# Kernel tuning notes

Measured on AMD Instinct MI355X. Metric: run time of the kernel, lower is better.

Reference implementation:

```python
import jax, jax.numpy as jnp
import numpy as np

N_NODES = 10000
N_EDGES = 640000
D = 128            # node_dims == edge_dims
HID = 2 * D        # ff hidden
EPS = 1e-6


def _layernorm(x, g, b):
    mu = jnp.mean(x, axis=-1, keepdims=True)
    var = jnp.var(x, axis=-1, keepdims=True)
    return (x - mu) * jax.lax.rsqrt(var + EPS) * g + b


def setup_inputs() -> dict:
    key = jax.random.key(0)
    ks = jax.random.split(key, 16)
    def lin(k, fan_in, fan_out):
        lim = 1.0 / np.sqrt(fan_in)
        kw, kb = jax.random.split(k)
        W = jax.random.uniform(kw, (fan_in, fan_out), jnp.float32, -lim, lim)
        b = jax.random.uniform(kb, (fan_out,), jnp.float32, -lim, lim)
        return W, b
    x = jax.random.normal(ks[0], (N_NODES, D), jnp.float32)
    edge_index = jax.random.randint(ks[1], (2, N_EDGES), 0, N_NODES, jnp.int64)
    edge_attr = jax.random.normal(ks[2], (N_EDGES, D), jnp.float32)
    # message MLP: Linear(3D->D), ReLU, Linear(D->D), ReLU, Linear(D->D)
    W1, b1 = lin(ks[3], 3 * D, D)
    W2, b2 = lin(ks[4], D, D)
    W3, b3 = lin(ks[5], D, D)
    # feedforward: Linear(D->2D), ReLU, Linear(2D->D)
    F1, bf1 = lin(ks[6], D, HID)
    F2, bf2 = lin(ks[7], HID, D)
    g0 = jnp.ones((D,), jnp.float32); be0 = jnp.zeros((D,), jnp.float32)
    g1 = jnp.ones((D,), jnp.float32); be1 = jnp.zeros((D,), jnp.float32)
    return {"x": x, "edge_index": edge_index, "edge_attr": edge_attr,
            "W1": W1, "b1": b1, "W2": W2, "b2": b2, "W3": W3, "b3": b3,
            "F1": F1, "bf1": bf1, "F2": F2, "bf2": bf2,
            "g0": g0, "be0": be0, "g1": g1, "be1": be1}


def reference(x, edge_index, edge_attr, W1, b1, W2, b2, W3, b3,
              F1, bf1, F2, bf2, g0, be0, g1, be1):
    src = edge_index[0]  # j
    dst = edge_index[1]  # i
    # message: cat([h_V_i, edge_attr, h_V_j]) -> MLP  (E x 3D gather)
    m = jnp.concatenate([x[dst], edge_attr, x[src]], axis=-1)
    m = jax.nn.relu(m @ W1 + b1)
    m = jax.nn.relu(m @ W2 + b2)
    m = m @ W3 + b3  # [E, D]
    # scatter-mean over destination nodes
    sums = jax.ops.segment_sum(m, dst, num_segments=N_NODES)
    cnt = jax.ops.segment_sum(jnp.ones((N_EDGES,), m.dtype), dst, num_segments=N_NODES)
    dh = sums / jnp.maximum(cnt, 1.0)[:, None]
    # residual + norm (dropout is identity at inference)
    h = _layernorm(x + dh, g0, be0)
    # pointwise feedforward
    ff = jax.nn.relu(h @ F1 + bf1) @ F2 + bf2
    return _layernorm(h + ff, g1, be1)
```

## Files before the change

### kernel.cpp

```cpp
#include <hip/hip_runtime.h>


#define NE 640000
#define NN 10000
#define DD 128
#define HIDN 256
#define EPSF 1e-6f
#define TILES4 10
#define EBLK4 250

typedef __attribute__((ext_vector_type(8))) short short8;
typedef __attribute__((ext_vector_type(4))) float f32x4;

__device__ __forceinline__ unsigned short f2bf(float f) {
    union { float f; unsigned int u; } v; v.f = f;
    unsigned int r = v.u + 0x7FFFu + ((v.u >> 16) & 1u);
    return (unsigned short)(r >> 16);
}
__device__ __forceinline__ float bf2f(unsigned short h) {
    union { unsigned int u; float f; } v; v.u = ((unsigned int)h) << 16;
    return v.f;
}
__device__ __forceinline__ int swzcol(int row, int col) {
    return (((col >> 3) ^ (row & 7)) << 3) | (col & 7);
}
__device__ __forceinline__ const short8* frag(const unsigned short* buf,
                                              int row, int kc, int q) {
    int g = (kc * 4 + q) ^ (row & 7);
    return (const short8*)(buf + row * 128 + g * 8);
}

__global__ __launch_bounds__(256)
void prep_pq(const float* __restrict__ W1, const float* __restrict__ W2,
             const float* __restrict__ W3, const float* __restrict__ b1,
             const float* __restrict__ x,
             unsigned short* __restrict__ WT,
             unsigned short* __restrict__ Pp, unsigned short* __restrict__ Qp)
{
    const int t = threadIdx.x;
    if (blockIdx.x < 192) {
        int g = blockIdx.x * 256 + t;
        int layer = g >> 14, r = g & 16383;
        int n = r >> 7, k = r & 127;
        const float* W = (layer == 0) ? (W1 + 128 * DD) : (layer == 1 ? W2 : W3);
        WT[layer * 16384 + n * 128 + swzcol(n, k)] = f2bf(W[k * DD + n]);
        return;
    }
    __shared__ float sx[16][DD];
    const int nb = (blockIdx.x - 192) * 16;

#pragma unroll
    for (int p = 0; p < 2; ++p) {
        int f = t + p * 256;
        int row = f >> 5, c4 = (f & 31) << 2;
        *(float4*)&sx[row][c4] = *(const float4*)(x + (long)(nb + row) * DD + c4);
    }
    __syncthreads();

    const int j  = t & 127;
    const int g8 = (t >> 7) << 3;
    const int pj = ((j & 15) << 3) + (j >> 4);

    for (int pass = 0; pass < 2; ++pass) {
        const float* W = W1 + (pass ? 256 * DD : 0);
        float acc[8];
#pragma unroll
        for (int v = 0; v < 8; ++v) acc[v] = 0.f;
        for (int k4 = 0; k4 < DD; k4 += 4) {
            float w0 = W[(k4 + 0) * DD + j];
            float w1 = W[(k4 + 1) * DD + j];
            float w2 = W[(k4 + 2) * DD + j];
            float w3 = W[(k4 + 3) * DD + j];
#pragma unroll
            for (int v = 0; v < 8; ++v) {
                float4 hv = *(const float4*)&sx[g8 + v][k4];
                acc[v] = fmaf(hv.x, w0, acc[v]);
                acc[v] = fmaf(hv.y, w1, acc[v]);
                acc[v] = fmaf(hv.z, w2, acc[v]);
                acc[v] = fmaf(hv.w, w3, acc[v]);
            }
        }
        unsigned short* Out = pass ? Qp : Pp;
        float bb = pass ? 0.f : b1[j];
#pragma unroll
        for (int v = 0; v < 8; ++v)
            Out[(long)(nb + g8 + v) * 128 + pj] = f2bf(acc[v] + bb);
    }
}

__global__ __launch_bounds__(512, 2)
void edge_mfma(const float* __restrict__ ea, const int* __restrict__ ei,
               const unsigned short* __restrict__ WT,
               const unsigned short* __restrict__ Pp,
               const unsigned short* __restrict__ Qp,
               const float* __restrict__ b2, const float* __restrict__ b3,
               float* __restrict__ sums, float* __restrict__ cnt)
{
    __shared__ unsigned short sW[3 * 16384];
    __shared__ unsigned short sAct[8 * 4096];

    const int t = threadIdx.x;
    const int wave = t >> 6, lane = t & 63;
    const int ln = lane & 15, q = lane >> 4;
    unsigned short* myA = sAct + wave * 4096;

    {
        const uint4* s = (const uint4*)WT;
        uint4* d = (uint4*)sW;
#pragma unroll
        for (int p = 0; p < 12; ++p) d[t + p * 512] = s[t + p * 512];
    }
    __syncthreads();

    float bv2[8], bv3[8];
#pragma unroll
    for (int ct = 0; ct < 8; ++ct) {
        bv2[ct] = b2[ct * 16 + ln];
        bv3[ct] = b3[ct * 16 + ln];
    }

    const long blkbase = (long)blockIdx.x * (TILES4 * 256);

    float4 Aq[16];
    int dstR[8], srcR[8];
    {
        long tb = blkbase;
#pragma unroll
        for (int rt = 0; rt < 2; ++rt)
#pragma unroll
            for (int kc = 0; kc < 4; ++kc) {
                long row = tb + wave * 32 + rt * 16 + ln;
                const float* p = ea + row * DD + kc * 32 + q * 8;
                Aq[rt * 8 + kc * 2 + 0] = *(const float4*)(p);
                Aq[rt * 8 + kc * 2 + 1] = *(const float4*)(p + 4);
            }
#pragma unroll
        for (int r = 0; r < 8; ++r) {
            long row = tb + wave * 32 + (r >> 2) * 16 + q * 4 + (r & 3);
            dstR[r] = ei[(long)NE + row];
            srcR[r] = ei[row];
        }
    }

    for (int it = 0; it < TILES4; ++it) {
        short8 af[2][4];
#pragma unroll
        for (int rt = 0; rt < 2; ++rt)
#pragma unroll
            for (int kc = 0; kc < 4; ++kc) {
                const float* f0 = (const float*)&Aq[rt * 8 + kc * 2];
                short8 v;
#pragma unroll
                for (int jj = 0; jj < 8; ++jj) v[jj] = (short)f2bf(f0[jj]);
                af[rt][kc] = v;
            }

        f32x4 acc[2][8];
#pragma unroll
        for (int r = 0; r < 8; ++r) {
            uint4 pv = *(const uint4*)(Pp + (long)dstR[r] * 128 + ln * 8);
            uint4 qv = *(const uint4*)(Qp + (long)srcR[r] * 128 + ln * 8);
            const unsigned short* pe = (const unsigned short*)&pv;
            const unsigned short* qe = (const unsigned short*)&qv;
#pragma unroll
            for (int ct = 0; ct < 8; ++ct)
                acc[r >> 2][ct][r & 3] = bf2f(pe[ct]) + bf2f(qe[ct]);
        }

        long nb_ = blkbase + (long)((it + 1 < TILES4) ? it + 1 : it) * 256;
        int ndst[8], nsrc[8];
#pragma unroll
        for (int rt = 0; rt < 2; ++rt)
#pragma unroll
            for (int kc = 0; kc < 4; ++kc) {
                long row = nb_ + wave * 32 + rt * 16 + ln;
                const float* p = ea + row * DD + kc * 32 + q * 8;
                Aq[rt * 8 + kc * 2 + 0] = *(const float4*)(p);
                Aq[rt * 8 + kc * 2 + 1] = *(const float4*)(p + 4);
            }
#pragma unroll
        for (int r = 0; r < 8; ++r) {
            long row = nb_ + wave * 32 + (r >> 2) * 16 + q * 4 + (r & 3);
            ndst[r] = ei[(long)NE + row];
            nsrc[r] = ei[row];
        }

#pragma unroll
        for (int kc = 0; kc < 4; ++kc)
#pragma unroll
            for (int ct = 0; ct < 8; ++ct) {
                short8 b = *frag(sW, ct * 16 + ln, kc, q);
                acc[0][ct] = __builtin_amdgcn_mfma_f32_16x16x32_bf16(af[0][kc], b, acc[0][ct], 0, 0, 0);
                acc[1][ct] = __builtin_amdgcn_mfma_f32_16x16x32_bf16(af[1][kc], b, acc[1][ct], 0, 0, 0);
            }
#pragma unroll
        for (int rt = 0; rt < 2; ++rt)
#pragma unroll
            for (int rg = 0; rg < 4; ++rg) {
                int row = rt * 16 + q * 4 + rg;
#pragma unroll
                for (int ct = 0; ct < 8; ++ct) {
                    int col = ct * 16 + ln;
                    myA[row * 128 + swzcol(row, col)] =
                        f2bf(fmaxf(acc[rt][ct][rg], 0.f));
                }
            }
        __builtin_amdgcn_wave_barrier();

#pragma unroll
        for (int rt = 0; rt < 2; ++rt)
#pragma unroll
            for (int ct = 0; ct < 8; ++ct) acc[rt][ct] = (f32x4)(0.f);
#pragma unroll
        for (int kc = 0; kc < 4; ++kc) {
            short8 a0 = *frag(myA, ln, kc, q);
            short8 a1 = *frag(myA, 16 + ln, kc, q);
#pragma unroll
            for (int ct = 0; ct < 8; ++ct) {
                short8 b = *frag(sW + 16384, ct * 16 + ln, kc, q);
                acc[0][ct] = __builtin_amdgcn_mfma_f32_16x16x32_bf16(a0, b, acc[0][ct], 0, 0, 0);
                acc[1][ct] = __builtin_amdgcn_mfma_f32_16x16x32_bf16(a1, b, acc[1][ct], 0, 0, 0);
            }
        }
        __builtin_amdgcn_wave_barrier();
#pragma unroll
        for (int rt = 0; rt < 2; ++rt)
#pragma unroll
            for (int rg = 0; rg < 4; ++rg) {
                int row = rt * 16 + q * 4 + rg;
#pragma unroll
                for (int ct = 0; ct < 8; ++ct) {
                    int col = ct * 16 + ln;
                    myA[row * 128 + swzcol(row, col)] =
                        f2bf(fmaxf(acc[rt][ct][rg] + bv2[ct], 0.f));
                }
            }
        __builtin_amdgcn_wave_barrier();

#pragma unroll
        for (int rt = 0; rt < 2; ++rt)
#pragma unroll
            for (int ct = 0; ct < 8; ++ct) acc[rt][ct] = (f32x4)(0.f);
#pragma unroll
        for (int kc = 0; kc < 4; ++kc) {
            short8 a0 = *frag(myA, ln, kc, q);
            short8 a1 = *frag(myA, 16 + ln, kc, q);
#pragma unroll
            for (int ct = 0; ct < 8; ++ct) {
                short8 b = *frag(sW + 32768, ct * 16 + ln, kc, q);
                acc[0][ct] = __builtin_amdgcn_mfma_f32_16x16x32_bf16(a0, b, acc[0][ct], 0, 0, 0);
                acc[1][ct] = __builtin_amdgcn_mfma_f32_16x16x32_bf16(a1, b, acc[1][ct], 0, 0, 0);
            }
        }
#pragma unroll
        for (int rt = 0; rt < 2; ++rt)
#pragma unroll
            for (int rg = 0; rg < 4; ++rg) {
                long dof = (long)dstR[rt * 4 + rg] * DD;
#pragma unroll
                for (int ct = 0; ct < 8; ++ct)
                    atomicAdd(sums + dof + ct * 16 + ln,
                              acc[rt][ct][rg] + bv3[ct]);
            }
        if (ln == 0) {
#pragma unroll
            for (int r = 0; r < 8; ++r) atomicAdd(cnt + dstR[r], 1.0f);
        }
#pragma unroll
        for (int r = 0; r < 8; ++r) { dstR[r] = ndst[r]; srcR[r] = nsrc[r]; }
    }
}

__global__ __launch_bounds__(256)
void node_fused(const float* __restrict__ x,
                const float* __restrict__ sums, const float* __restrict__ cnt,
                const float* __restrict__ F1, const float* __restrict__ bf1,
                const float* __restrict__ F2, const float* __restrict__ bf2,
                const float* __restrict__ g0, const float* __restrict__ be0,
                const float* __restrict__ g1, const float* __restrict__ be1,
                float* __restrict__ out)
{
    constexpr int NPB = 8;
    __shared__ float sh[NPB][DD];
    __shared__ float shid[NPB][HIDN];
    __shared__ float sz[NPB][DD];

    const int t = threadIdx.x;
    const int wave = t >> 6, lane = t & 63;
    const int half = lane >> 5, l2 = lane & 31;
    const int nl = wave * 2 + half;
    const int node = blockIdx.x * NPB + nl;
    const long base = (long)node * DD;

    float inv = 1.0f / fmaxf(cnt[node], 1.0f);
    float y[4], s = 0.f, ss = 0.f;
#pragma unroll
    for (int e = 0; e < 4; ++e) {
        int c = l2 + 32 * e;
        y[e] = x[base + c] + sums[base + c] * inv;
        s += y[e]; ss += y[e] * y[e];
    }
#pragma unroll
    for (int off = 16; off > 0; off >>= 1) {
        s += __shfl_down(s, off, 32); ss += __shfl_down(ss, off, 32);
    }
    s = __shfl(s, 0, 32); ss = __shfl(ss, 0, 32);
    float mean = s * (1.0f / DD);
    float var  = ss * (1.0f / DD) - mean * mean;
    float rstd = rsqrtf(var + EPSF);
#pragma unroll
    for (int e = 0; e < 4; ++e) {
        int c = l2 + 32 * e;
        sh[nl][c] = (y[e] - mean) * rstd * g0[c] + be0[c];
    }
    __syncthreads();

    float hacc[NPB];
    float bb = bf1[t];
#pragma unroll
    for (int v = 0; v < NPB; ++v) hacc[v] = bb;
    for (int k4 = 0; k4 < DD; k4 += 4) {
        float w0 = F1[(long)(k4 + 0) * HIDN + t];
        float w1 = F1[(long)(k4 + 1) * HIDN + t];
        float w2 = F1[(long)(k4 + 2) * HIDN + t];
        float w3 = F1[(long)(k4 + 3) * HIDN + t];
#pragma unroll
        for (int v = 0; v < NPB; ++v) {
            float4 hv = *(const float4*)&sh[v][k4];
            hacc[v] = fmaf(hv.x, w0, hacc[v]);
            hacc[v] = fmaf(hv.y, w1, hacc[v]);
            hacc[v] = fmaf(hv.z, w2, hacc[v]);
            hacc[v] = fmaf(hv.w, w3, hacc[v]);
        }
    }
#pragma unroll
    for (int v = 0; v < NPB; ++v) shid[v][t] = fmaxf(hacc[v], 0.f);
    __syncthreads();

    const int col = t & (DD - 1);
    const int grp = (t >> 7) * 4;
    float o[4];
#pragma unroll
    for (int v = 0; v < 4; ++v) o[v] = bf2[col];
    for (int k4 = 0; k4 < HIDN; k4 += 4) {
        float w0 = F2[(long)(k4 + 0) * DD + col];
        float w1 = F2[(long)(k4 + 1) * DD + col];
        float w2 = F2[(long)(k4 + 2) * DD + col];
        float w3 = F2[(long)(k4 + 3) * DD + col];
#pragma unroll
        for (int v = 0; v < 4; ++v) {
            float4 hv = *(const float4*)&shid[grp + v][k4];
            o[v] = fmaf(hv.x, w0, o[v]);
            o[v] = fmaf(hv.y, w1, o[v]);
            o[v] = fmaf(hv.z, w2, o[v]);
            o[v] = fmaf(hv.w, w3, o[v]);
        }
    }
#pragma unroll
    for (int v = 0; v < 4; ++v) sz[grp + v][col] = sh[grp + v][col] + o[v];
    __syncthreads();

    float z[4]; s = 0.f; ss = 0.f;
#pragma unroll
    for (int e = 0; e < 4; ++e) {
        int c = l2 + 32 * e;
        z[e] = sz[nl][c]; s += z[e]; ss += z[e] * z[e];
    }
#pragma unroll
    for (int off = 16; off > 0; off >>= 1) {
        s += __shfl_down(s, off, 32); ss += __shfl_down(ss, off, 32);
    }
    s = __shfl(s, 0, 32); ss = __shfl(ss, 0, 32);
    mean = s * (1.0f / DD);
    var  = ss * (1.0f / DD) - mean * mean;
    rstd = rsqrtf(var + EPSF);
#pragma unroll
    for (int e = 0; e < 4; ++e) {
        int c = l2 + 32 * e;
        out[base + c] = (z[e] - mean) * rstd * g1[c] + be1[c];
    }
}

extern "C" void kernel_launch(void* const* d_in, const int* in_sizes, int n_in,
                              void* d_out, int out_size, void* d_ws, size_t ws_size,
                              hipStream_t stream)
{
    const float* x   = (const float*)d_in[0];
    const int*   ei  = (const int*)  d_in[1];
    const float* ea  = (const float*)d_in[2];
    const float* W1  = (const float*)d_in[3];
    const float* b1  = (const float*)d_in[4];
    const float* W2  = (const float*)d_in[5];
    const float* b2  = (const float*)d_in[6];
    const float* W3  = (const float*)d_in[7];
    const float* b3  = (const float*)d_in[8];
    const float* F1  = (const float*)d_in[9];
    const float* bf1 = (const float*)d_in[10];
    const float* F2  = (const float*)d_in[11];
    const float* bf2 = (const float*)d_in[12];
    const float* g0  = (const float*)d_in[13];
    const float* be0 = (const float*)d_in[14];
    const float* g1  = (const float*)d_in[15];
    const float* be1 = (const float*)d_in[16];
    float* out = (float*)d_out;

    char* ws = (char*)d_ws;
    float*          sums = (float*)(ws);
    float*          cnt  = (float*)(ws + 5120000);
    unsigned short* WT   = (unsigned short*)(ws + 5160192);
    unsigned short* Pp   = (unsigned short*)(ws + 5258752);
    unsigned short* Qp   = (unsigned short*)(ws + 7818752);

    hipMemsetAsync(ws, 0, 5160000, stream);
    prep_pq<<<192 + NN / 16, 256, 0, stream>>>(W1, W2, W3, b1, x, WT, Pp, Qp);
    edge_mfma<<<EBLK4, 512, 0, stream>>>(ea, ei, WT, Pp, Qp, b2, b3, sums, cnt);
    node_fused<<<NN / 8, 256, 0, stream>>>(x, sums, cnt, F1, bf1, F2, bf2,
                                           g0, be0, g1, be1, out);
}
```

Measured before the change: 807.9 us.

## Sort edges by destination and merge consecutive same-destination atomics

Adds a counting sort of edges by destination (histogram, single-block scan, scatter) and has the edge kernel process edges in sorted order, gathering edge_attr rows through a permutation. Within each 4-row MFMA fragment group, runs of equal destination are summed in registers before one atomicAdd, and the separate count atomics are replaced by the histogram. The P/Q addition moves into the first-layer epilogue, with the edge features staged through LDS. The goal is less atomic contention and traffic, in exchange for three extra kernel launches, a serial scan, and edge_attr reads that are no longer contiguous.

```diff
diff --git a/kernel.cpp b/kernel.cpp
--- a/kernel.cpp
+++ b/kernel.cpp
@@ -6,8 +6,8 @@
 #define DD 128
 #define HIDN 256
 #define EPSF 1e-6f
-#define TILES4 10
-#define EBLK4 250
+#define TILES5 10
+#define EBLK5 250
 
 typedef __attribute__((ext_vector_type(8))) short short8;
 typedef __attribute__((ext_vector_type(4))) float f32x4;
@@ -57,9 +57,9 @@
     }
     __syncthreads();
 
-    const int j  = t & 127;
+    const int s  = t & 127;
+    const int j  = ((s & 7) << 4) | (s >> 3);
     const int g8 = (t >> 7) << 3;
-    const int pj = ((j & 15) << 3) + (j >> 4);
 
     for (int pass = 0; pass < 2; ++pass) {
         const float* W = W1 + (pass ? 256 * DD : 0);
@@ -84,17 +84,67 @@
         float bb = pass ? 0.f : b1[j];
 #pragma unroll
         for (int v = 0; v < 8; ++v)
-            Out[(long)(nb + g8 + v) * 128 + pj] = f2bf(acc[v] + bb);
-    }
+            Out[(long)(nb + g8 + v) * 128 + s] = f2bf(acc[v] + bb);
+    }
+}
+
+__global__ __launch_bounds__(256)
+void hist_kernel(const int* __restrict__ ei, int* __restrict__ hist)
+{
+    int e = blockIdx.x * 256 + threadIdx.x;
+    atomicAdd(hist + ei[(long)NE + e], 1);
+}
+
+__global__ __launch_bounds__(256)
+void scan_kernel(const int* __restrict__ hist, int* __restrict__ ofs)
+{
+    __shared__ int wsum[4];
+    __shared__ int carry;
+    const int t = threadIdx.x, w = t >> 6, l = t & 63;
+    if (t == 0) carry = 0;
+    __syncthreads();
+    for (int base = 0; base < NN; base += 256) {
+        int v = (base + t < NN) ? hist[base + t] : 0;
+        int inc = v;
+#pragma unroll
+        for (int off = 1; off < 64; off <<= 1) {
+            int u = __shfl_up(inc, off);
+            if (l >= off) inc += u;
+        }
+        if (l == 63) wsum[w] = inc;
+        __syncthreads();
+        int add = 0;
+        for (int i = 0; i < 4; ++i) if (i < w) add += wsum[i];
+        if (base + t < NN) ofs[base + t] = carry + add + inc - v;
+        __syncthreads();
+        if (t == 255) carry += wsum[0] + wsum[1] + wsum[2] + wsum[3];
+        __syncthreads();
+    }
+}
+
+__global__ __launch_bounds__(256)
+void scatter_kernel(const int* __restrict__ ei, int* __restrict__ ofs,
+                    int* __restrict__ permE, int* __restrict__ permSrc,
+                    int* __restrict__ permDst)
+{
+    int e = blockIdx.x * 256 + threadIdx.x;
+    int sN = ei[e];
+    int d  = ei[(long)NE + e];
+    int pos = atomicAdd(ofs + d, 1);
+    permE[pos]   = e;
+    permSrc[pos] = sN;
+    permDst[pos] = d;
 }
 
 __global__ __launch_bounds__(512, 2)
-void edge_mfma(const float* __restrict__ ea, const int* __restrict__ ei,
+void edge_mfma(const float* __restrict__ ea,
+               const int* __restrict__ permE, const int* __restrict__ permSrc,
+               const int* __restrict__ permDst,
                const unsigned short* __restrict__ WT,
                const unsigned short* __restrict__ Pp,
                const unsigned short* __restrict__ Qp,
                const float* __restrict__ b2, const float* __restrict__ b3,
-               float* __restrict__ sums, float* __restrict__ cnt)
+               float* __restrict__ sums)
 {
     __shared__ unsigned short sW[3 * 16384];
     __shared__ unsigned short sAct[8 * 4096];
@@ -102,6 +152,7 @@
     const int t = threadIdx.x;
     const int wave = t >> 6, lane = t & 63;
     const int ln = lane & 15, q = lane >> 4;
+    const int hi = lane >> 5, lo = lane & 31;
     unsigned short* myA = sAct + wave * 4096;
 
     {
@@ -112,6 +163,10 @@
     }
     __syncthreads();
 
+    int rowoff[8];
+#pragma unroll
+    for (int r = 0; r < 8; ++r) rowoff[r] = (r >> 2) * 16 + q * 4 + (r & 3);
+
     float bv2[8], bv3[8];
 #pragma unroll
     for (int ct = 0; ct < 8; ++ct) {
@@ -119,92 +174,87 @@
         bv3[ct] = b3[ct * 16 + ln];
     }
 
-    const long blkbase = (long)blockIdx.x * (TILES4 * 256);
-
+    const long blkbase = (long)blockIdx.x * (TILES5 * 256);
+    const int r0g = wave * 32;
+
+    int prow[16], dstR[8], srcR[8];
     float4 Aq[16];
-    int dstR[8], srcR[8];
     {
-        long tb = blkbase;
+        long tb = blkbase + r0g;
+#pragma unroll
+        for (int jj = 0; jj < 16; ++jj) prow[jj] = permE[tb + 2 * jj + hi];
+#pragma unroll
+        for (int r = 0; r < 8; ++r) {
+            dstR[r] = permDst[tb + rowoff[r]];
+            srcR[r] = permSrc[tb + rowoff[r]];
+        }
+#pragma unroll
+        for (int jj = 0; jj < 16; ++jj)
+            Aq[jj] = *(const float4*)(ea + (long)prow[jj] * DD + lo * 4);
+    }
+
+    for (int it = 0; it < TILES5; ++it) {
+        uint4 pv[8], qv[8];
+#pragma unroll
+        for (int r = 0; r < 8; ++r) {
+            pv[r] = *(const uint4*)(Pp + (long)dstR[r] * 128 + ln * 8);
+            qv[r] = *(const uint4*)(Qp + (long)srcR[r] * 128 + ln * 8);
+        }
+
+#pragma unroll
+        for (int jj = 0; jj < 16; ++jj) {
+            int srow = 2 * jj + hi, c4 = lo * 4;
+            float4 v = Aq[jj];
+            uint2 pk;
+            pk.x = (unsigned)f2bf(v.x) | ((unsigned)f2bf(v.y) << 16);
+            pk.y = (unsigned)f2bf(v.z) | ((unsigned)f2bf(v.w) << 16);
+            *(uint2*)(myA + srow * 128 + swzcol(srow, c4)) = pk;
+        }
+        __builtin_amdgcn_wave_barrier();
+
+        long nb = blkbase + (long)((it + 1 < TILES5) ? it + 1 : it) * 256 + r0g;
+        int nprow[16], ndst[8], nsrc[8];
+#pragma unroll
+        for (int jj = 0; jj < 16; ++jj) nprow[jj] = permE[nb + 2 * jj + hi];
+#pragma unroll
+        for (int r = 0; r < 8; ++r) {
+            ndst[r] = permDst[nb + rowoff[r]];
+            nsrc[r] = permSrc[nb + rowoff[r]];
+        }
+
+        f32x4 acc[2][8];
 #pragma unroll
         for (int rt = 0; rt < 2; ++rt)
 #pragma unroll
-            for (int kc = 0; kc < 4; ++kc) {
-                long row = tb + wave * 32 + rt * 16 + ln;
-                const float* p = ea + row * DD + kc * 32 + q * 8;
-                Aq[rt * 8 + kc * 2 + 0] = *(const float4*)(p);
-                Aq[rt * 8 + kc * 2 + 1] = *(const float4*)(p + 4);
-            }
-#pragma unroll
-        for (int r = 0; r < 8; ++r) {
-            long row = tb + wave * 32 + (r >> 2) * 16 + q * 4 + (r & 3);
-            dstR[r] = ei[(long)NE + row];
-            srcR[r] = ei[row];
-        }
-    }
-
-    for (int it = 0; it < TILES4; ++it) {
-        short8 af[2][4];
-#pragma unroll
-        for (int rt = 0; rt < 2; ++rt)
-#pragma unroll
-            for (int kc = 0; kc < 4; ++kc) {
-                const float* f0 = (const float*)&Aq[rt * 8 + kc * 2];
-                short8 v;
-#pragma unroll
-                for (int jj = 0; jj < 8; ++jj) v[jj] = (short)f2bf(f0[jj]);
-                af[rt][kc] = v;
-            }
-
-        f32x4 acc[2][8];
-#pragma unroll
-        for (int r = 0; r < 8; ++r) {
-            uint4 pv = *(const uint4*)(Pp + (long)dstR[r] * 128 + ln * 8);
-            uint4 qv = *(const uint4*)(Qp + (long)srcR[r] * 128 + ln * 8);
-            const unsigned short* pe = (const unsigned short*)&pv;
-            const unsigned short* qe = (const unsigned short*)&qv;
-#pragma unroll
-            for (int ct = 0; ct < 8; ++ct)
-                acc[r >> 2][ct][r & 3] = bf2f(pe[ct]) + bf2f(qe[ct]);
-        }
-
-        long nb_ = blkbase + (long)((it + 1 < TILES4) ? it + 1 : it) * 256;
-        int ndst[8], nsrc[8];
-#pragma unroll
-        for (int rt = 0; rt < 2; ++rt)
-#pragma unroll
-            for (int kc = 0; kc < 4; ++kc) {
-                long row = nb_ + wave * 32 + rt * 16 + ln;
-                const float* p = ea + row * DD + kc * 32 + q * 8;
-                Aq[rt * 8 + kc * 2 + 0] = *(const float4*)(p);
-                Aq[rt * 8 + kc * 2 + 1] = *(const float4*)(p + 4);
-            }
-#pragma unroll
-        for (int r = 0; r < 8; ++r) {
-            long row = nb_ + wave * 32 + (r >> 2) * 16 + q * 4 + (r & 3);
-            ndst[r] = ei[(long)NE + row];
-            nsrc[r] = ei[row];
-        }
-
-#pragma unroll
-        for (int kc = 0; kc < 4; ++kc)
+            for (int ct = 0; ct < 8; ++ct) acc[rt][ct] = (f32x4)(0.f);
+#pragma unroll
+        for (int kc = 0; kc < 4; ++kc) {
+            short8 a0 = *frag(myA, ln, kc, q);
+            short8 a1 = *frag(myA, 16 + ln, kc, q);
 #pragma unroll
             for (int ct = 0; ct < 8; ++ct) {
                 short8 b = *frag(sW, ct * 16 + ln, kc, q);
-                acc[0][ct] = __builtin_amdgcn_mfma_f32_16x16x32_bf16(af[0][kc], b, acc[0][ct], 0, 0, 0);
-                acc[1][ct] = __builtin_amdgcn_mfma_f32_16x16x32_bf16(af[1][kc], b, acc[1][ct], 0, 0, 0);
-            }
-#pragma unroll
-        for (int rt = 0; rt < 2; ++rt)
-#pragma unroll
-            for (int rg = 0; rg < 4; ++rg) {
-                int row = rt * 16 + q * 4 + rg;
-#pragma unroll
-                for (int ct = 0; ct < 8; ++ct) {
-                    int col = ct * 16 + ln;
-                    myA[row * 128 + swzcol(row, col)] =
-                        f2bf(fmaxf(acc[rt][ct][rg], 0.f));
-                }
-            }
+                acc[0][ct] = __builtin_amdgcn_mfma_f32_16x16x32_bf16(a0, b, acc[0][ct], 0, 0, 0);
+                acc[1][ct] = __builtin_amdgcn_mfma_f32_16x16x32_bf16(a1, b, acc[1][ct], 0, 0, 0);
+            }
+        }
+
+#pragma unroll
+        for (int jj = 0; jj < 16; ++jj)
+            Aq[jj] = *(const float4*)(ea + (long)nprow[jj] * DD + lo * 4);
+
+        __builtin_amdgcn_wave_barrier();
+#pragma unroll
+        for (int r = 0; r < 8; ++r) {
+            const unsigned short* pe = (const unsigned short*)&pv[r];
+            const unsigned short* qe = (const unsigned short*)&qv[r];
+            int row = rowoff[r];
+#pragma unroll
+            for (int ct = 0; ct < 8; ++ct) {
+                float v = acc[r >> 2][ct][r & 3] + bf2f(pe[ct]) + bf2f(qe[ct]);
+                myA[row * 128 + swzcol(row, ct * 16 + ln)] = f2bf(fmaxf(v, 0.f));
+            }
+        }
         __builtin_amdgcn_wave_barrier();
 
 #pragma unroll
@@ -224,17 +274,14 @@
         }
         __builtin_amdgcn_wave_barrier();
 #pragma unroll
-        for (int rt = 0; rt < 2; ++rt)
-#pragma unroll
-            for (int rg = 0; rg < 4; ++rg) {
-                int row = rt * 16 + q * 4 + rg;
-#pragma unroll
-                for (int ct = 0; ct < 8; ++ct) {
-                    int col = ct * 16 + ln;
-                    myA[row * 128 + swzcol(row, col)] =
-                        f2bf(fmaxf(acc[rt][ct][rg] + bv2[ct], 0.f));
-                }
-            }
+        for (int r = 0; r < 8; ++r) {
+            int row = rowoff[r];
+#pragma unroll
+            for (int ct = 0; ct < 8; ++ct) {
+                float v = fmaxf(acc[r >> 2][ct][r & 3] + bv2[ct], 0.f);
+                myA[row * 128 + swzcol(row, ct * 16 + ln)] = f2bf(v);
+            }
+        }
         __builtin_amdgcn_wave_barrier();
 
 #pragma unroll
@@ -252,20 +299,44 @@
                 acc[1][ct] = __builtin_amdgcn_mfma_f32_16x16x32_bf16(a1, b, acc[1][ct], 0, 0, 0);
             }
         }
+
 #pragma unroll
         for (int rt = 0; rt < 2; ++rt)
 #pragma unroll
-            for (int rg = 0; rg < 4; ++rg) {
-                long dof = (long)dstR[rt * 4 + rg] * DD;
-#pragma unroll
-                for (int ct = 0; ct < 8; ++ct)
-                    atomicAdd(sums + dof + ct * 16 + ln,
-                              acc[rt][ct][rg] + bv3[ct]);
-            }
-        if (ln == 0) {
-#pragma unroll
-            for (int r = 0; r < 8; ++r) atomicAdd(cnt + dstR[r], 1.0f);
-        }
+            for (int ct = 0; ct < 8; ++ct)
+#pragma unroll
+                for (int rg = 0; rg < 4; ++rg)
+                    acc[rt][ct][rg] += bv3[ct];
+#pragma unroll
+        for (int rt = 0; rt < 2; ++rt) {
+            int d = dstR[rt * 4];
+            float run[8];
+#pragma unroll
+            for (int ct = 0; ct < 8; ++ct) run[ct] = acc[rt][ct][0];
+#pragma unroll
+            for (int rg = 1; rg < 4; ++rg) {
+                int dn = dstR[rt * 4 + rg];
+                if (dn == d) {
+#pragma unroll
+                    for (int ct = 0; ct < 8; ++ct) run[ct] += acc[rt][ct][rg];
+                } else {
+                    long o = (long)d * DD;
+#pragma unroll
+                    for (int ct = 0; ct < 8; ++ct)
+                        atomicAdd(sums + o + ct * 16 + ln, run[ct]);
+                    d = dn;
+#pragma unroll
+                    for (int ct = 0; ct < 8; ++ct) run[ct] = acc[rt][ct][rg];
+                }
+            }
+            long o = (long)d * DD;
+#pragma unroll
+            for (int ct = 0; ct < 8; ++ct)
+                atomicAdd(sums + o + ct * 16 + ln, run[ct]);
+        }
+
+#pragma unroll
+        for (int jj = 0; jj < 16; ++jj) prow[jj] = nprow[jj];
 #pragma unroll
         for (int r = 0; r < 8; ++r) { dstR[r] = ndst[r]; srcR[r] = nsrc[r]; }
     }
@@ -273,7 +344,7 @@
 
 __global__ __launch_bounds__(256)
 void node_fused(const float* __restrict__ x,
-                const float* __restrict__ sums, const float* __restrict__ cnt,
+                const float* __restrict__ sums, const int* __restrict__ hist,
                 const float* __restrict__ F1, const float* __restrict__ bf1,
                 const float* __restrict__ F2, const float* __restrict__ bf2,
                 const float* __restrict__ g0, const float* __restrict__ be0,
@@ -292,7 +363,7 @@
     const int node = blockIdx.x * NPB + nl;
     const long base = (long)node * DD;
 
-    float inv = 1.0f / fmaxf(cnt[node], 1.0f);
+    float inv = 1.0f / fmaxf((float)hist[node], 1.0f);
     float y[4], s = 0.f, ss = 0.f;
 #pragma unroll
     for (int e = 0; e < 4; ++e) {
@@ -405,15 +476,23 @@
     float* out = (float*)d_out;
 
     char* ws = (char*)d_ws;
-    float*          sums = (float*)(ws);
-    float*          cnt  = (float*)(ws + 5120000);
-    unsigned short* WT   = (unsigned short*)(ws + 5160192);
-    unsigned short* Pp   = (unsigned short*)(ws + 5258752);
-    unsigned short* Qp   = (unsigned short*)(ws + 7818752);
+    float*          sums    = (float*)(ws);
+    int*            hist    = (int*)  (ws + 5120000);
+    unsigned short* WT      = (unsigned short*)(ws + 5160192);
+    unsigned short* Pp      = (unsigned short*)(ws + 5258752);
+    unsigned short* Qp      = (unsigned short*)(ws + 7818752);
+    int*            ofs     = (int*)  (ws + 10378752);
+    int*            permE   = (int*)  (ws + 10418944);
+    int*            permSrc = (int*)  (ws + 12978944);
+    int*            permDst = (int*)  (ws + 15538944);
 
     hipMemsetAsync(ws, 0, 5160000, stream);
     prep_pq<<<192 + NN / 16, 256, 0, stream>>>(W1, W2, W3, b1, x, WT, Pp, Qp);
-    edge_mfma<<<EBLK4, 512, 0, stream>>>(ea, ei, WT, Pp, Qp, b2, b3, sums, cnt);
-    node_fused<<<NN / 8, 256, 0, stream>>>(x, sums, cnt, F1, bf1, F2, bf2,
+    hist_kernel<<<NE / 256, 256, 0, stream>>>(ei, hist);
+    scan_kernel<<<1, 256, 0, stream>>>(hist, ofs);
+    scatter_kernel<<<NE / 256, 256, 0, stream>>>(ei, ofs, permE, permSrc, permDst);
+    edge_mfma<<<EBLK5, 512, 0, stream>>>(ea, permE, permSrc, permDst,
+                                         WT, Pp, Qp, b2, b3, sums);
+    node_fused<<<NN / 8, 256, 0, stream>>>(x, sums, hist, F1, bf1, F2, bf2,
                                            g0, be0, g1, be1, out);
 }
```

New measurement: 1.048 ms. 1.3x slower.
